# Kernel optimization log

Measured on AMD Instinct MI355X. Metric: run time of the kernel, lower is better.

The kernel has to match this reference:

```python
import jax, jax.numpy as jnp
import numpy as np

B, S, IN, OUT, RANK, LORA_R = 2, 2048, 4096, 4096, 8, 16
LORA_SCALING = 16.0 / LORA_R  # alpha / r = 1.0


def setup_inputs() -> dict:
    key = jax.random.key(0)
    ks = jax.random.split(key, 6)
    x = jax.random.normal(ks[0], (B, S, IN), dtype=jnp.float32)
    weight = jax.random.normal(ks[1], (OUT, IN), dtype=jnp.float32) * 0.02  # Q (snapped weights)
    scale_A = jax.random.normal(ks[2], (OUT, RANK), dtype=jnp.float32) * 0.1
    scale_B = jax.random.normal(ks[3], (RANK, IN), dtype=jnp.float32) * 0.1
    rank_magnitude = jnp.ones((RANK,), dtype=jnp.float32)
    lora_A = jax.random.normal(ks[4], (LORA_R, IN), dtype=jnp.float32) * 0.02
    lora_B = jax.random.normal(ks[5], (OUT, LORA_R), dtype=jnp.float32) * 0.02
    return {"x": x, "weight": weight, "scale_A": scale_A, "scale_B": scale_B,
            "rank_magnitude": rank_magnitude, "lora_A": lora_A, "lora_B": lora_B}


def reference(x, weight, scale_A, scale_B, rank_magnitude, lora_A, lora_B):
    # y_o = sum_k g_k * a_{ok} * sum_i Q_{oi} * b_{ki} * x_i
    #     = sum_i (Q_{oi} * sum_k (g_k a_{ok}) b_{ki}) x_i
    # i.e. a single dense GEMM with the precomputed effective weight
    # W_eff = Q * ((scale_A * g) @ scale_B)  -- same math, rank dim folded once.
    S_mat = jnp.einsum('ok,ki->oi', scale_A * rank_magnitude[None, :], scale_B)  # [out, in]
    W_eff = weight * S_mat                                                        # [out, in]
    y = jnp.einsum('bsi,oi->bso', x, W_eff)                                       # [B, S, out]
    # LoRA add: (x @ A^T) @ B^T * scaling
    y = y + ((x @ lora_A.T) @ lora_B.T) * LORA_SCALING
    return y
```

## Files before the change

kernel.cpp:

```cpp
#include <hip/hip_runtime.h>

#define M_DIM 4096
#define IN_DIM 4096
#define OUT_DIM 4096
#define RANK 8
#define LORA_R 16
#define LORA_SCALING 1.0f

typedef __bf16 bf16;
typedef bf16  bf16x4 __attribute__((ext_vector_type(4)));
typedef bf16  bf16x8 __attribute__((ext_vector_type(8)));
typedef float f32x4  __attribute__((ext_vector_type(4)));
typedef float f32x16 __attribute__((ext_vector_type(16)));

#define OG 8
__global__ __launch_bounds__(256) void prep_fused(
    const float* __restrict__ weight, const float* __restrict__ scale_A,
    const float* __restrict__ scale_B, const float* __restrict__ g,
    const float* __restrict__ lora_A, const float* __restrict__ lora_B,
    const float* __restrict__ x, bf16* __restrict__ wt, bf16* __restrict__ xb)
{
    const int t = threadIdx.x;
    if (blockIdx.x < 2048) {
        __shared__ float s_sa[OG][RANK];
        __shared__ float s_lb[OG][LORA_R];
        const int o0 = (blockIdx.x >> 2) * OG;
        if (t < OG * RANK) {
            int r8 = t / RANK, k = t % RANK;
            s_sa[r8][k] = scale_A[(o0 + r8) * RANK + k] * g[k];
        }
        if (t < OG * LORA_R) {
            int r8 = t / LORA_R, r = t % LORA_R;
            s_lb[r8][r] = lora_B[(o0 + r8) * LORA_R + r] * LORA_SCALING;
        }
        __syncthreads();

        const int i0 = ((blockIdx.x & 3) * 256 + t) * 4;

        f32x4 acc[OG];
#pragma unroll
        for (int r8 = 0; r8 < OG; ++r8) acc[r8] = {0.f, 0.f, 0.f, 0.f};
#pragma unroll
        for (int k = 0; k < RANK; ++k) {
            f32x4 sbk = *(const f32x4*)(scale_B + k * IN_DIM + i0);
#pragma unroll
            for (int r8 = 0; r8 < OG; ++r8) acc[r8] += s_sa[r8][k] * sbk;
        }
#pragma unroll
        for (int r8 = 0; r8 < OG; ++r8) {
            f32x4 wv = *(const f32x4*)(weight + (size_t)(o0 + r8) * IN_DIM + i0);
            acc[r8] *= wv;
        }
#pragma unroll
        for (int r = 0; r < LORA_R; ++r) {
            f32x4 lak = *(const f32x4*)(lora_A + r * IN_DIM + i0);
#pragma unroll
            for (int r8 = 0; r8 < OG; ++r8) acc[r8] += s_lb[r8][r] * lak;
        }
#pragma unroll
        for (int r8 = 0; r8 < OG; ++r8) {
            bf16x4 h = { (bf16)acc[r8][0], (bf16)acc[r8][1],
                         (bf16)acc[r8][2], (bf16)acc[r8][3] };
            *(bf16x4*)(wt + (size_t)(o0 + r8) * IN_DIM + i0) = h;
        }
    } else {
        const int n4  = (M_DIM * IN_DIM) / 4;
        int idx    = (blockIdx.x - 2048) * 256 + t;
        int stride = 2048 * 256;
        for (int i = idx; i < n4; i += stride) {
            f32x4 v = *(const f32x4*)(x + (size_t)i * 4);
            bf16x4 h = { (bf16)v[0], (bf16)v[1], (bf16)v[2], (bf16)v[3] };
            *(bf16x4*)(xb + (size_t)i * 4) = h;
        }
    }
}

#define BM 128
#define BN 128
#define BK 32

__device__ __forceinline__ void gload_lds16(const bf16* g, bf16* l) {
    __builtin_amdgcn_global_load_lds(
        (const __attribute__((address_space(1))) void*)g,
        (__attribute__((address_space(3))) void*)l,
        16, 0, 0);
}

__global__ __launch_bounds__(256) void gemm_bt(
    const bf16* __restrict__ A,
    const bf16* __restrict__ Bw,
    float* __restrict__ C)
{
    __shared__ __align__(16) char smem[16896];
    bf16* sA = (bf16*)smem;
    bf16* sB = (bf16*)(smem + 8192);

    const int t    = threadIdx.x;
    const int w    = t >> 6;
    const int lane = t & 63;
    const int lh   = lane >> 5;
    const int ln   = lane & 31;

    const int bid = blockIdx.x;
    const int xcd = bid & 7;
    const int rr_ = bid >> 3;
    const int m0  = (xcd * 4 + (rr_ & 3)) * BM;
    const int n0  = (rr_ >> 2) * BN;

    const int wm = (w >> 1) * 64;
    const int wn = (w & 1) * 64;

    const int srow = t >> 2;
    const int scol = ((t & 3) ^ ((t >> 3) & 3)) * 8;
    const bf16* gA0 = A  + (size_t)(m0 + srow)      * IN_DIM + scol;
    const bf16* gA1 = A  + (size_t)(m0 + 64 + srow) * IN_DIM + scol;
    const bf16* gB0 = Bw + (size_t)(n0 + srow)      * IN_DIM + scol;
    const bf16* gB1 = Bw + (size_t)(n0 + 64 + srow) * IN_DIM + scol;
    bf16* lA0 = sA + w * 512;
    bf16* lA1 = sA + 2048 + w * 512;
    bf16* lB0 = sB + w * 512;
    bf16* lB1 = sB + 2048 + w * 512;

    const bf16* pA[2][2];
    const bf16* pB[2][2];
#pragma unroll
    for (int tm = 0; tm < 2; ++tm) {
        int rowA = wm + tm * 32 + ln;
        int rowB = wn + tm * 32 + ln;
#pragma unroll
        for (int s = 0; s < 2; ++s) {
            pA[tm][s] = sA + rowA * 32 + (((s * 2 + lh) ^ ((rowA >> 1) & 3)) * 8);
            pB[tm][s] = sB + rowB * 32 + (((s * 2 + lh) ^ ((rowB >> 1) & 3)) * 8);
        }
    }

    f32x16 acc[2][2] = {};

    for (int k0 = 0; k0 < IN_DIM; k0 += BK) {
        __syncthreads();
        gload_lds16(gA0 + k0, lA0);
        gload_lds16(gA1 + k0, lA1);
        gload_lds16(gB0 + k0, lB0);
        gload_lds16(gB1 + k0, lB1);
        __syncthreads();

        bf16x8 af[2][2], bf_[2][2];
#pragma unroll
        for (int tm = 0; tm < 2; ++tm)
#pragma unroll
            for (int s = 0; s < 2; ++s) {
                af[tm][s]  = *(const bf16x8*)pA[tm][s];
                bf_[tm][s] = *(const bf16x8*)pB[tm][s];
            }
#pragma unroll
        for (int s = 0; s < 2; ++s)
#pragma unroll
            for (int tm = 0; tm < 2; ++tm)
#pragma unroll
                for (int tn = 0; tn < 2; ++tn)
                    acc[tm][tn] = __builtin_amdgcn_mfma_f32_32x32x16_bf16(
                        af[tm][s], bf_[tn][s], acc[tm][tn], 0, 0, 0);
    }

    __syncthreads();
    float* sEw = (float*)smem + w * (32 * 33);
#pragma unroll
    for (int tm = 0; tm < 2; ++tm)
#pragma unroll
        for (int tn = 0; tn < 2; ++tn) {
#pragma unroll
            for (int j = 0; j < 16; ++j) {
                int row = (j & 3) + 8 * (j >> 2) + 4 * lh;
                sEw[row * 33 + ln] = acc[tm][tn][j];
            }
#pragma unroll
            for (int p = 0; p < 4; ++p) {
                int r4 = p * 8 + (lane >> 3);
                int c4 = (lane & 7) * 4;
                f32x4 v = { sEw[r4 * 33 + c4],     sEw[r4 * 33 + c4 + 1],
                            sEw[r4 * 33 + c4 + 2], sEw[r4 * 33 + c4 + 3] };
                *(f32x4*)(C + (size_t)(m0 + wm + tm * 32 + r4) * OUT_DIM
                            + (n0 + wn + tn * 32 + c4)) = v;
            }
        }
}

extern "C" void kernel_launch(void* const* d_in, const int* in_sizes, int n_in,
                              void* d_out, int out_size, void* d_ws, size_t ws_size,
                              hipStream_t stream) {
    (void)in_sizes; (void)n_in; (void)out_size; (void)ws_size;
    const float* x        = (const float*)d_in[0];
    const float* weight   = (const float*)d_in[1];
    const float* scale_A  = (const float*)d_in[2];
    const float* scale_B  = (const float*)d_in[3];
    const float* g        = (const float*)d_in[4];
    const float* lora_A   = (const float*)d_in[5];
    const float* lora_B   = (const float*)d_in[6];
    float* out = (float*)d_out;

    bf16* xb = (bf16*)d_ws;
    bf16* wt = (bf16*)((char*)d_ws + (size_t)M_DIM * IN_DIM * sizeof(bf16));

    prep_fused<<<4096, 256, 0, stream>>>(weight, scale_A, scale_B, g,
                                         lora_A, lora_B, x, wt, xb);

    gemm_bt<<<(M_DIM / BM) * (OUT_DIM / BN), 256, 0, stream>>>(xb, wt, out);
}
```

Before: 340.6 us.

## Rewrite GEMM as 256x256 tiled, 8-wave double-buffered pipeline with interleaved loads

```diff
diff --git a/kernel.cpp b/kernel.cpp
--- a/kernel.cpp
+++ b/kernel.cpp
@@ -75,112 +75,173 @@
     }
 }
 
-#define BM 128
-#define BN 128
-#define BK 32
-
-__device__ __forceinline__ void gload_lds16(const bf16* g, bf16* l) {
+#define BM 256
+#define BN 256
+#define BK 64
+
+__device__ __forceinline__ void gload16(const bf16* g, bf16* l) {
     __builtin_amdgcn_global_load_lds(
         (const __attribute__((address_space(1))) void*)g,
         (__attribute__((address_space(3))) void*)l,
         16, 0, 0);
 }
 
-__global__ __launch_bounds__(256) void gemm_bt(
+#define MFMA(d, a, b) d = __builtin_amdgcn_mfma_f32_32x32x16_bf16((a), (b), (d), 0, 0, 0)
+#define BARRIER() __builtin_amdgcn_s_barrier()
+#define WAIT_LGKM0() asm volatile("s_waitcnt lgkmcnt(0)" ::: "memory")
+#define WAIT_VM(n)   asm volatile("s_waitcnt vmcnt(" #n ")" ::: "memory")
+
+__global__ __launch_bounds__(512, 2) void gemm_bt(
     const bf16* __restrict__ A,
     const bf16* __restrict__ Bw,
     float* __restrict__ C)
 {
-    __shared__ __align__(16) char smem[16896];
-    bf16* sA = (bf16*)smem;
-    bf16* sB = (bf16*)(smem + 8192);
-
-    const int t    = threadIdx.x;
-    const int w    = t >> 6;
-    const int lane = t & 63;
-    const int lh   = lane >> 5;
-    const int ln   = lane & 31;
+    __shared__ __align__(16) char smem[131072];
+
+    const int t  = threadIdx.x;
+    const int w  = t >> 6;
+    const int l  = t & 63;
+    const int lh = l >> 5;
+    const int ln = l & 31;
+    const int wm = w >> 2;
+    const int wn = w & 3;
 
     const int bid = blockIdx.x;
     const int xcd = bid & 7;
-    const int rr_ = bid >> 3;
-    const int m0  = (xcd * 4 + (rr_ & 3)) * BM;
-    const int n0  = (rr_ >> 2) * BN;
-
-    const int wm = (w >> 1) * 64;
-    const int wn = (w & 1) * 64;
-
-    const int srow = t >> 2;
-    const int scol = ((t & 3) ^ ((t >> 3) & 3)) * 8;
-    const bf16* gA0 = A  + (size_t)(m0 + srow)      * IN_DIM + scol;
-    const bf16* gA1 = A  + (size_t)(m0 + 64 + srow) * IN_DIM + scol;
-    const bf16* gB0 = Bw + (size_t)(n0 + srow)      * IN_DIM + scol;
-    const bf16* gB1 = Bw + (size_t)(n0 + 64 + srow) * IN_DIM + scol;
-    bf16* lA0 = sA + w * 512;
-    bf16* lA1 = sA + 2048 + w * 512;
-    bf16* lB0 = sB + w * 512;
-    bf16* lB1 = sB + 2048 + w * 512;
-
-    const bf16* pA[2][2];
-    const bf16* pB[2][2];
-#pragma unroll
-    for (int tm = 0; tm < 2; ++tm) {
-        int rowA = wm + tm * 32 + ln;
-        int rowB = wn + tm * 32 + ln;
-#pragma unroll
-        for (int s = 0; s < 2; ++s) {
-            pA[tm][s] = sA + rowA * 32 + (((s * 2 + lh) ^ ((rowA >> 1) & 3)) * 8);
-            pB[tm][s] = sB + rowB * 32 + (((s * 2 + lh) ^ ((rowB >> 1) & 3)) * 8);
-        }
+    const int loc = bid >> 3;
+    const int mt  = (xcd & 3) * 4 + (loc >> 3);
+    const int nt  = (xcd >> 2) * 8 + (loc & 7);
+    const int m0  = mt * BM;
+    const int n0  = nt * BN;
+
+    const int srow   = l >> 2;
+    const int schunk = (l & 3) ^ ((l >> 3) & 3);
+    const size_t soff = (size_t)(w * 16 + srow) * IN_DIM + schunk * 8;
+    const bf16* gA = A  + (size_t)m0 * IN_DIM + soff;
+    const bf16* gB = Bw + (size_t)n0 * IN_DIM + soff;
+    const int wA = w << 10;
+
+#define STAGE(gsrc, dstbyte) do {                                   \
+        bf16* d_ = (bf16*)(smem + (dstbyte));                       \
+        gload16((gsrc), d_);                                        \
+        gload16((gsrc) + (size_t)128 * IN_DIM, d_ + 4096);          \
+    } while (0)
+
+    const int s4  = (ln >> 1) & 3;
+    const int cEv = ((lh)     ^ s4) << 4;
+    const int cOd = ((2 + lh) ^ s4) << 4;
+    const char* aB0 = smem + (wm * 128 + ln) * 64;
+    const char* bB0 = smem + 65536 + (wn * 64 + ln) * 64;
+
+    f32x16 acc[4][2] = {};
+
+    STAGE(gA + 0,  0      + wA);
+    STAGE(gB + 0,  65536  + wA);
+    STAGE(gA + 32, 16384  + wA);
+    STAGE(gB + 32, 65536 + 16384 + wA);
+    STAGE(gA + 64, 32768  + wA);
+    STAGE(gB + 64, 65536 + 32768 + wA);
+    WAIT_VM(4);
+    BARRIER();
+
+#pragma unroll 2
+    for (int kt = 0; kt < 64; ++kt) {
+        const int p   = kt & 1;
+        const int po  = p << 15;
+        const int qo  = po ^ 32768;
+        const int kc1 = (kt + 1 < 64) ? (kt + 1) * BK : 0;
+        const int kc2 = (kt + 2 < 64) ? (kt + 2) * BK : 0;
+
+        bf16x8 a00 = *(const bf16x8*)(aB0 + po + cEv);
+        bf16x8 a01 = *(const bf16x8*)(aB0 + po + cOd);
+        bf16x8 a10 = *(const bf16x8*)(aB0 + po + 2048 + cEv);
+        bf16x8 a11 = *(const bf16x8*)(aB0 + po + 2048 + cOd);
+        bf16x8 b00 = *(const bf16x8*)(bB0 + po + cEv);
+        bf16x8 b01 = *(const bf16x8*)(bB0 + po + cOd);
+        bf16x8 b10 = *(const bf16x8*)(bB0 + po + 2048 + cEv);
+        bf16x8 b11 = *(const bf16x8*)(bB0 + po + 2048 + cOd);
+        STAGE(gA + kc1 + 32, qo + 16384 + wA);
+        BARRIER();
+        WAIT_LGKM0();
+        __builtin_amdgcn_s_setprio(1);
+        MFMA(acc[0][0], a00, b00); MFMA(acc[0][1], a00, b10);
+        MFMA(acc[1][0], a10, b00); MFMA(acc[1][1], a10, b10);
+        MFMA(acc[0][0], a01, b01); MFMA(acc[0][1], a01, b11);
+        MFMA(acc[1][0], a11, b01); MFMA(acc[1][1], a11, b11);
+        __builtin_amdgcn_s_setprio(0);
+        BARRIER();
+
+        bf16x8 a20 = *(const bf16x8*)(aB0 + po + 4096 + cEv);
+        bf16x8 a21 = *(const bf16x8*)(aB0 + po + 4096 + cOd);
+        bf16x8 a30 = *(const bf16x8*)(aB0 + po + 6144 + cEv);
+        bf16x8 a31 = *(const bf16x8*)(aB0 + po + 6144 + cOd);
+        STAGE(gB + kc1 + 32, 65536 + qo + 16384 + wA);
+        BARRIER();
+        WAIT_LGKM0();
+        __builtin_amdgcn_s_setprio(1);
+        MFMA(acc[2][0], a20, b00); MFMA(acc[2][1], a20, b10);
+        MFMA(acc[3][0], a30, b00); MFMA(acc[3][1], a30, b10);
+        MFMA(acc[2][0], a21, b01); MFMA(acc[2][1], a21, b11);
+        MFMA(acc[3][0], a31, b01); MFMA(acc[3][1], a31, b11);
+        __builtin_amdgcn_s_setprio(0);
+        BARRIER();
+
+        a00 = *(const bf16x8*)(aB0 + po + 16384 + cEv);
+        a01 = *(const bf16x8*)(aB0 + po + 16384 + cOd);
+        a10 = *(const bf16x8*)(aB0 + po + 16384 + 2048 + cEv);
+        a11 = *(const bf16x8*)(aB0 + po + 16384 + 2048 + cOd);
+        b00 = *(const bf16x8*)(bB0 + po + 16384 + cEv);
+        b01 = *(const bf16x8*)(bB0 + po + 16384 + cOd);
+        b10 = *(const bf16x8*)(bB0 + po + 16384 + 2048 + cEv);
+        b11 = *(const bf16x8*)(bB0 + po + 16384 + 2048 + cOd);
+        STAGE(gA + kc2, po + wA);
+        BARRIER();
+        WAIT_LGKM0();
+        __builtin_amdgcn_s_setprio(1);
+        MFMA(acc[0][0], a00, b00); MFMA(acc[0][1], a00, b10);
+        MFMA(acc[1][0], a10, b00); MFMA(acc[1][1], a10, b10);
+        MFMA(acc[0][0], a01, b01); MFMA(acc[0][1], a01, b11);
+        MFMA(acc[1][0], a11, b01); MFMA(acc[1][1], a11, b11);
+        __builtin_amdgcn_s_setprio(0);
+        BARRIER();
+
+        a20 = *(const bf16x8*)(aB0 + po + 16384 + 4096 + cEv);
+        a21 = *(const bf16x8*)(aB0 + po + 16384 + 4096 + cOd);
+        a30 = *(const bf16x8*)(aB0 + po + 16384 + 6144 + cEv);
+        a31 = *(const bf16x8*)(aB0 + po + 16384 + 6144 + cOd);
+        STAGE(gB + kc2, 65536 + po + wA);
+        BARRIER();
+        WAIT_LGKM0();
+        __builtin_amdgcn_s_setprio(1);
+        MFMA(acc[2][0], a20, b00); MFMA(acc[2][1], a20, b10);
+        MFMA(acc[3][0], a30, b00); MFMA(acc[3][1], a30, b10);
+        MFMA(acc[2][0], a21, b01); MFMA(acc[2][1], a21, b11);
+        MFMA(acc[3][0], a31, b01); MFMA(acc[3][1], a31, b11);
+        __builtin_amdgcn_s_setprio(0);
+        WAIT_VM(4);
+        BARRIER();
     }
 
-    f32x16 acc[2][2] = {};
-
-    for (int k0 = 0; k0 < IN_DIM; k0 += BK) {
-        __syncthreads();
-        gload_lds16(gA0 + k0, lA0);
-        gload_lds16(gA1 + k0, lA1);
-        gload_lds16(gB0 + k0, lB0);
-        gload_lds16(gB1 + k0, lB1);
-        __syncthreads();
-
-        bf16x8 af[2][2], bf_[2][2];
-#pragma unroll
-        for (int tm = 0; tm < 2; ++tm)
-#pragma unroll
-            for (int s = 0; s < 2; ++s) {
-                af[tm][s]  = *(const bf16x8*)pA[tm][s];
-                bf_[tm][s] = *(const bf16x8*)pB[tm][s];
-            }
-#pragma unroll
-        for (int s = 0; s < 2; ++s)
-#pragma unroll
-            for (int tm = 0; tm < 2; ++tm)
-#pragma unroll
-                for (int tn = 0; tn < 2; ++tn)
-                    acc[tm][tn] = __builtin_amdgcn_mfma_f32_32x32x16_bf16(
-                        af[tm][s], bf_[tn][s], acc[tm][tn], 0, 0, 0);
-    }
-
-    __syncthreads();
-    float* sEw = (float*)smem + w * (32 * 33);
-#pragma unroll
-    for (int tm = 0; tm < 2; ++tm)
-#pragma unroll
-        for (int tn = 0; tn < 2; ++tn) {
+    asm volatile("s_waitcnt vmcnt(0) lgkmcnt(0)" ::: "memory");
+    BARRIER();
+    float* sEw = (float*)(void*)smem + w * (32 * 33);
+#pragma unroll
+    for (int tm2 = 0; tm2 < 4; ++tm2)
+#pragma unroll
+        for (int tn2 = 0; tn2 < 2; ++tn2) {
 #pragma unroll
             for (int j = 0; j < 16; ++j) {
                 int row = (j & 3) + 8 * (j >> 2) + 4 * lh;
-                sEw[row * 33 + ln] = acc[tm][tn][j];
+                sEw[row * 33 + ln] = acc[tm2][tn2][j];
             }
 #pragma unroll
-            for (int p = 0; p < 4; ++p) {
-                int r4 = p * 8 + (lane >> 3);
-                int c4 = (lane & 7) * 4;
+            for (int q = 0; q < 4; ++q) {
+                int r4 = q * 8 + (l >> 3);
+                int c4 = (l & 7) * 4;
                 f32x4 v = { sEw[r4 * 33 + c4],     sEw[r4 * 33 + c4 + 1],
                             sEw[r4 * 33 + c4 + 2], sEw[r4 * 33 + c4 + 3] };
-                *(f32x4*)(C + (size_t)(m0 + wm + tm * 32 + r4) * OUT_DIM
-                            + (n0 + wn + tn * 32 + c4)) = v;
+                *(f32x4*)(C + (size_t)(m0 + wm * 128 + tm2 * 32 + r4) * OUT_DIM
+                            + (n0 + wn * 64 + tn2 * 32 + c4)) = v;
             }
         }
 }
@@ -204,5 +265,5 @@
     prep_fused<<<4096, 256, 0, stream>>>(weight, scale_A, scale_B, g,
                                          lora_A, lora_B, x, wt, xb);
 
-    gemm_bt<<<(M_DIM / BM) * (OUT_DIM / BN), 256, 0, stream>>>(xb, wt, out);
-}
+    gemm_bt<<<(M_DIM / BM) * (OUT_DIM / BN), 512, 0, stream>>>(xb, wt, out);
+}
```

Result: faster. 307.8 us (-9.6%).
